# Performance work log

Measured on AMD Instinct MI355X. Metric: run time of the kernel, lower is better.

## Reference

```python
import jax, jax.numpy as jnp
import numpy as np

INPUT, HIDDEN, OUTPUT, BATCH = 2048, 32, 512, 16384


def setup_inputs() -> dict:
    key = jax.random.key(0)
    k1, k2, k3, k4 = jax.random.split(key, 4)
    x = jax.random.normal(k1, (BATCH, INPUT), dtype=jnp.float32)
    # torch init: uniform(-1, 1) for both linear weights and hebbian coeffs
    w1 = jax.random.uniform(k2, (HIDDEN, INPUT), jnp.float32, -1.0, 1.0)
    w2 = jax.random.uniform(k3, (OUTPUT, HIDDEN), jnp.float32, -1.0, 1.0)
    heb_coeffs = jax.random.uniform(k4, (HIDDEN * INPUT + OUTPUT * HIDDEN, 4), jnp.float32, -1.0, 1.0)
    return {"x": x, "w1": w1, "w2": w2, "heb_coeffs": heb_coeffs}


def reference(x, w1, w2, heb_coeffs):
    # Forward MLP: act = relu(x @ w1^T), out = sigmoid(act @ w2^T) - 0.4
    act = jax.nn.relu(x @ w1.T)                 # [B, HIDDEN]
    out = jax.nn.sigmoid(act @ w2.T) - 0.4      # [B, OUTPUT]

    B = x.shape[0]
    # idx = (shape0-1)*i + i + j == shape0*i + j  -> coeff layout [in_dim, out_dim, 4]
    c1 = heb_coeffs[: HIDDEN * INPUT].reshape(INPUT, HIDDEN, 4)
    c2 = heb_coeffs[HIDDEN * INPUT :].reshape(HIDDEN, OUTPUT, 4)

    # ABCD update, batch loop -> batch-summed outer products / rank-1 terms
    corr1 = jnp.einsum("bi,bj->ij", x, act)     # [INPUT, HIDDEN]
    dw1T = (B * c1[..., 3]
            + c1[..., 0] * corr1
            + c1[..., 1] * x.sum(0)[:, None]
            + c1[..., 2] * act.sum(0)[None, :])  # [INPUT, HIDDEN]

    corr2 = jnp.einsum("bi,bj->ij", act, out)   # [HIDDEN, OUTPUT]
    dw2T = (B * c2[..., 3]
            + c2[..., 0] * corr2
            + c2[..., 1] * act.sum(0)[:, None]
            + c2[..., 2] * out.sum(0)[None, :])  # [HIDDEN, OUTPUT]

    w1_new = w1 + dw1T.T                        # [HIDDEN, INPUT]
    w2_new = w2 + dw2T.T                        # [OUTPUT, HIDDEN]
    # row-wise L2 normalization (torch.norm(dim=1, keepdim=True))
    w1_new = w1_new / jnp.linalg.norm(w1_new, axis=1, keepdims=True)
    w2_new = w2_new / jnp.linalg.norm(w2_new, axis=1, keepdims=True)
    return out, w1_new, w2_new
```

## Files before the change

### kernel.cpp

```cpp
#include <hip/hip_runtime.h>
#include <math.h>

constexpr int BATCH = 16384;
constexpr int IND   = 2048;
constexpr int HID   = 32;
constexpr int OUTD  = 512;

constexpr int NC1 = 64;
constexpr int NSA = 64;
constexpr int NC2 = 128;

constexpr int SA   = 136;
constexpr int SXT  = 72;
constexpr int SATW = 136;
constexpr int SAT2 = 264;

typedef __attribute__((ext_vector_type(8))) short bf16x8;
typedef __attribute__((ext_vector_type(4))) float f32x4;

__device__ __forceinline__ unsigned short f2bf(float f) {
  unsigned u = __float_as_uint(f);
  u += 0x7FFFu + ((u >> 16) & 1u);
  return (unsigned short)(u >> 16);
}
__device__ __forceinline__ float bf2f(unsigned short h) {
  return __uint_as_float(((unsigned)h) << 16);
}
__device__ __forceinline__ void split2(float f, unsigned short& hi,
                                       unsigned short& lo) {
  hi = f2bf(f);
  lo = f2bf(f - bf2f(hi));
}
__device__ __forceinline__ int swzA(int row, int col) {
  return row * SA + (col ^ (((row >> 3) & 7) * 8));
}

__global__ __launch_bounds__(256) void k_cvtw(
    const float* __restrict__ w1, const float* __restrict__ w2,
    unsigned short* __restrict__ w1H, unsigned short* __restrict__ w1L,
    unsigned short* __restrict__ w2H, unsigned short* __restrict__ w2L) {
  const int bid = blockIdx.x;
  if (bid < 64) {
    const int g = bid * 256 + threadIdx.x;
    float4 v = ((const float4*)w1)[g];
    ushort4 h, l;
    split2(v.x, h.x, l.x); split2(v.y, h.y, l.y);
    split2(v.z, h.z, l.z); split2(v.w, h.w, l.w);
    ((ushort4*)w1H)[g] = h;
    ((ushort4*)w1L)[g] = l;
  } else {
    const int g = (bid - 64) * 256 + threadIdx.x;
    float4 v = ((const float4*)w2)[g];
    ushort4 h, l;
    split2(v.x, h.x, l.x); split2(v.y, h.y, l.y);
    split2(v.z, h.z, l.z); split2(v.w, h.w, l.w);
    ((ushort4*)w2H)[g] = h;
    ((ushort4*)w2L)[g] = l;
  }
}

__global__ __launch_bounds__(256, 4) void k_act(
    const float* __restrict__ x, const unsigned short* __restrict__ w1H,
    const unsigned short* __restrict__ w1L, float* __restrict__ act_part,
    unsigned short* __restrict__ xH) {
  const int tid = threadIdx.x;
  const int kq = blockIdx.x & 1;
  const int bt = blockIdx.x >> 1;
  const int b0 = bt * 32;
  const int kbase = kq * 1024;
  const int lane = tid & 63;
  const int wv = tid >> 6;
  const int arow = lane & 15;
  const int m4 = lane >> 4;
  const int ksub = m4 * 8;
  const int rt = wv & 1;
  const int ht = wv >> 1;

  __shared__ __align__(16) unsigned short XH[32 * SA];
  __shared__ __align__(16) unsigned short XL[32 * SA];
  __shared__ __align__(16) unsigned short WH[32 * SA];
  __shared__ __align__(16) unsigned short WL[32 * SA];

  const int rp = tid >> 4;
  const int kg = (tid & 15) * 8;

  float4 px0a, px0b, px1a, px1b;
  bf16x8 pwh0, pwl0, pwh1, pwl1;

#define LOADA(K0)                                                          \
  {                                                                        \
    const float* xr0 = x + (size_t)(b0 + 2 * rp) * IND + kbase + (K0) + kg;\
    const float* xr1 = xr0 + IND;                                          \
    px0a = *(const float4*)(xr0);                                          \
    px0b = *(const float4*)(xr0 + 4);                                      \
    px1a = *(const float4*)(xr1);                                          \
    px1b = *(const float4*)(xr1 + 4);                                      \
    const size_t wo = (size_t)(2 * rp) * IND + kbase + (K0) + kg;          \
    pwh0 = *(const bf16x8*)(&w1H[wo]);                                     \
    pwl0 = *(const bf16x8*)(&w1L[wo]);                                     \
    pwh1 = *(const bf16x8*)(&w1H[wo + IND]);                               \
    pwl1 = *(const bf16x8*)(&w1L[wo + IND]);                               \
  }

#define PUTX2(ROW, COL, V, GK)                                       \
  {                                                                  \
    ushort4 h_, l_;                                                  \
    split2((V).x, h_.x, l_.x); split2((V).y, h_.y, l_.y);            \
    split2((V).z, h_.z, l_.z); split2((V).w, h_.w, l_.w);            \
    *(ushort4*)(&XH[swzA((ROW), (COL))]) = h_;                       \
    *(ushort4*)(&XL[swzA((ROW), (COL))]) = l_;                       \
    *(ushort4*)(&xH[(size_t)(b0 + (ROW)) * IND + (GK) + (COL)]) = h_;\
  }

#define STOREA(GK)                                                   \
  {                                                                  \
    PUTX2(2 * rp, kg, px0a, GK);                                     \
    PUTX2(2 * rp, kg + 4, px0b, GK);                                 \
    PUTX2(2 * rp + 1, kg, px1a, GK);                                 \
    PUTX2(2 * rp + 1, kg + 4, px1b, GK);                             \
    *(bf16x8*)(&WH[swzA(2 * rp, kg)]) = pwh0;                        \
    *(bf16x8*)(&WL[swzA(2 * rp, kg)]) = pwl0;                        \
    *(bf16x8*)(&WH[swzA(2 * rp + 1, kg)]) = pwh1;                    \
    *(bf16x8*)(&WL[swzA(2 * rp + 1, kg)]) = pwl1;                    \
  }

  f32x4 accA = {0.f, 0.f, 0.f, 0.f};
  LOADA(0);

  for (int kc = 0; kc < 8; ++kc) {
    __syncthreads();
    STOREA(kbase + kc * 128);
    __syncthreads();
    if (kc < 7) LOADA((kc + 1) * 128);
    const int xrow = rt * 16 + arow;
    const int wrow = ht * 16 + arow;
#pragma unroll
    for (int ks = 0; ks < 4; ++ks) {
      const int kk = ks * 32 + ksub;
      bf16x8 ah = *(const bf16x8*)(&XH[swzA(xrow, kk)]);
      bf16x8 al = *(const bf16x8*)(&XL[swzA(xrow, kk)]);
      bf16x8 bh = *(const bf16x8*)(&WH[swzA(wrow, kk)]);
      bf16x8 bl_ = *(const bf16x8*)(&WL[swzA(wrow, kk)]);
      accA = __builtin_amdgcn_mfma_f32_16x16x32_bf16(ah, bh, accA, 0, 0, 0);
      accA = __builtin_amdgcn_mfma_f32_16x16x32_bf16(ah, bl_, accA, 0, 0, 0);
      accA = __builtin_amdgcn_mfma_f32_16x16x32_bf16(al, bh, accA, 0, 0, 0);
    }
  }

  const int bl = rt * 16 + (m4 << 2);
  const int h = ht * 16 + arow;
  float* p = act_part + (size_t)kq * (BATCH * HID);
#pragma unroll
  for (int r = 0; r < 4; ++r)
    p[(size_t)(b0 + bl + r) * HID + h] = accA[r];
}

__global__ __launch_bounds__(256) void k_actc(
    const float* __restrict__ act_part,
    unsigned short* __restrict__ actH, unsigned short* __restrict__ actL,
    unsigned short* __restrict__ actT, float* __restrict__ actsum_part) {
  const int tid = threadIdx.x;
  const int blk = blockIdx.x;
  const int b0 = blk * 256;

  __shared__ unsigned short asT[32][264];
  __shared__ float red[256][4];

  const float4* p0 = (const float4*)act_part;
  const float4* p1 = p0 + (size_t)BATCH * HID / 4;

  const int hq = tid & 7;
  float4 s{0.f, 0.f, 0.f, 0.f};
#pragma unroll
  for (int r = 0; r < 8; ++r) {
    const int e4 = r * 256 + tid;
    const int b = e4 >> 3;
    const size_t g = (size_t)(b0 + b) * 8 + hq;
    float4 a = p0[g];
    float4 c = p1[g];
    a.x = fmaxf(a.x + c.x, 0.f);  a.y = fmaxf(a.y + c.y, 0.f);
    a.z = fmaxf(a.z + c.z, 0.f);  a.w = fmaxf(a.w + c.w, 0.f);
    ushort4 hh, ll;
    split2(a.x, hh.x, ll.x); split2(a.y, hh.y, ll.y);
    split2(a.z, hh.z, ll.z); split2(a.w, hh.w, ll.w);
    *(ushort4*)(&actH[g * 4]) = hh;
    *(ushort4*)(&actL[g * 4]) = ll;
    asT[hq * 4 + 0][b] = hh.x;
    asT[hq * 4 + 1][b] = hh.y;
    asT[hq * 4 + 2][b] = hh.z;
    asT[hq * 4 + 3][b] = hh.w;
    s.x += a.x; s.y += a.y; s.z += a.z; s.w += a.w;
  }
  red[tid][0] = s.x; red[tid][1] = s.y;
  red[tid][2] = s.z; red[tid][3] = s.w;
  __syncthreads();

#pragma unroll
  for (int r = 0; r < 4; ++r) {
    const int slot = r * 256 + tid;
    const int hrow = slot >> 5;
    const int bseg = (slot & 31) * 8;
    bf16x8 v = *(const bf16x8*)(&asT[hrow][bseg]);
    *(bf16x8*)(&actT[(size_t)hrow * BATCH + b0 + bseg]) = v;
  }
  if (tid < 32) {
    const int q = tid >> 2, j = tid & 3;
    float t = 0.f;
#pragma unroll
    for (int sx = 0; sx < 32; ++sx) t += red[q + 8 * sx][j];
    actsum_part[blk * HID + tid] = t;
  }
}

__global__ __launch_bounds__(512, 3) void k_corr1(
    const unsigned short* __restrict__ xH,
    const unsigned short* __restrict__ actT,
    float* __restrict__ corr1T_part, float* __restrict__ xsum_part) {
  const int tid = threadIdx.x;
  const int bc = blockIdx.x >> 4;
  const int iq = blockIdx.x & 15;
  const int b0 = bc * 256;
  const int ibase = iq * 128;
  const int lane = tid & 63;
  const int wv = tid >> 6;
  const int arow = lane & 15;
  const int m4 = lane >> 4;
  const int ksub = m4 * 8;
  const int it = wv * 16;

  __shared__ __align__(16) unsigned short XT[128 * SXT];
  __shared__ __align__(16) unsigned short AT[48 * SAT2];

  for (int e = tid; e < 16 * SAT2; e += 512)
    AT[32 * SAT2 + e] = (unsigned short)0x3F80;
  {
    const int hrow = tid >> 4;
    const int sg = (tid & 15) * 16;
    const int sw = ((hrow >> 3) & 7) * 8;
#pragma unroll
    for (int j = 0; j < 2; ++j) {
      const int boff = sg + 8 * j;
      bf16x8 v = *(const bf16x8*)(&actT[(size_t)hrow * BATCH + b0 + boff]);
      *(bf16x8*)(&AT[hrow * SAT2 + (boff ^ sw)]) = v;
    }
  }

  const int ig = tid & 15;
  const int bq = tid >> 4;

  bf16x8 xa, ya;

#define LOADC(HF)                                                           \
  {                                                                         \
    const int icol = ibase + ig * 8;                                        \
    const unsigned short* r0 =                                              \
        xH + (size_t)(b0 + 64 * (HF) + 2 * bq) * IND + icol;                \
    xa = *(const bf16x8*)(r0);                                              \
    ya = *(const bf16x8*)(r0 + IND);                                        \
  }

#define STC                                                                 \
  {                                                                         \
    const int qb = (2 * bq) ^ ((ig & 7) * 8);                               \
    unsigned short* basew = &XT[(size_t)(ig * 8) * SXT + qb];               \
    ushort2 p;                                                              \
    p.x = (unsigned short)xa[0]; p.y = (unsigned short)ya[0];               \
    *(ushort2*)(basew + 0 * SXT) = p;                                       \
    p.x = (unsigned short)xa[1]; p.y = (unsigned short)ya[1];               \
    *(ushort2*)(basew + 1 * SXT) = p;                                       \
    p.x = (unsigned short)xa[2]; p.y = (unsigned short)ya[2];               \
    *(ushort2*)(basew + 2 * SXT) = p;                                       \
    p.x = (unsigned short)xa[3]; p.y = (unsigned short)ya[3];               \
    *(ushort2*)(basew + 3 * SXT) = p;                                       \
    p.x = (unsigned short)xa[4]; p.y = (unsigned short)ya[4];               \
    *(ushort2*)(basew + 4 * SXT) = p;                                       \
    p.x = (unsigned short)xa[5]; p.y = (unsigned short)ya[5];               \
    *(ushort2*)(basew + 5 * SXT) = p;                                       \
    p.x = (unsigned short)xa[6]; p.y = (unsigned short)ya[6];               \
    *(ushort2*)(basew + 6 * SXT) = p;                                       \
    p.x = (unsigned short)xa[7]; p.y = (unsigned short)ya[7];               \
    *(ushort2*)(basew + 7 * SXT) = p;                                       \
  }

  const int swzr = (((it + arow) >> 3) & 7) * 8;
  const int swze0 = ((arow >> 3) & 7) * 8;
  const int swze1 = (((16 + arow) >> 3) & 7) * 8;

  f32x4 c00 = {0.f, 0.f, 0.f, 0.f};
  f32x4 c01 = {0.f, 0.f, 0.f, 0.f};
  f32x4 c02 = {0.f, 0.f, 0.f, 0.f};

  LOADC(0);
#pragma unroll
  for (int hf = 0; hf < 4; ++hf) {
    __syncthreads();
    STC;
    __syncthreads();
    if (hf < 3) LOADC(hf + 1);
#pragma unroll
    for (int bs = 0; bs < 2; ++bs) {
      const int bb = bs * 32 + ksub;
      const int bb2 = 64 * hf + bb;
      bf16x8 a = *(const bf16x8*)(&XT[(it + arow) * SXT + (bb ^ swzr)]);
      bf16x8 e0 = *(const bf16x8*)(&AT[arow * SAT2 + (bb2 ^ swze0)]);
      bf16x8 e1 = *(const bf16x8*)(&AT[(16 + arow) * SAT2 + (bb2 ^ swze1)]);
      bf16x8 e2 = *(const bf16x8*)(&AT[(32 + arow) * SAT2 + bb2]);
      c00 = __builtin_amdgcn_mfma_f32_16x16x32_bf16(a, e0, c00, 0, 0, 0);
      c01 = __builtin_amdgcn_mfma_f32_16x16x32_bf16(a, e1, c01, 0, 0, 0);
      c02 = __builtin_amdgcn_mfma_f32_16x16x32_bf16(a, e2, c02, 0, 0, 0);
    }
  }

  float* basep = corr1T_part + (size_t)bc * (IND * HID);
  const int gi = ibase + it + (m4 << 2);
  *(f32x4*)(basep + (size_t)arow * IND + gi) = c00;
  *(f32x4*)(basep + (size_t)(16 + arow) * IND + gi) = c01;
  if (arow == 0)
    *(f32x4*)(xsum_part + (size_t)bc * IND + gi) = c02;
}

__global__ __launch_bounds__(256, 2) void k_fwd2m_red1(
    const unsigned short* __restrict__ actH,
    const unsigned short* __restrict__ actL,
    const unsigned short* __restrict__ actT,
    const unsigned short* __restrict__ w2H,
    const unsigned short* __restrict__ w2L,
    float* __restrict__ out, float* __restrict__ corr2_part,
    float* __restrict__ outsum_part,
    const float* __restrict__ c1p, const float* __restrict__ xsp,
    const float* __restrict__ asp,
    float* __restrict__ corr1T, float* __restrict__ xsum,
    float* __restrict__ actsum) {
  __shared__ __align__(16) unsigned short W2Hs[128 * 40];
  __shared__ __align__(16) unsigned short W2Ls[128 * 40];
  __shared__ __align__(16) unsigned short AH[64 * 40];
  __shared__ __align__(16) unsigned short AL[64 * 40];
  __shared__ __align__(16) unsigned short AT[48 * SATW];
  __shared__ __align__(16) unsigned short OT[128 * 72];

  const int tid = threadIdx.x;

  if (blockIdx.x >= 512) {
    const int e = (blockIdx.x - 512) * 256 + tid;
    float s = 0.f;
#pragma unroll 8
    for (int c = 0; c < NC1; ++c) s += c1p[(size_t)c * (IND * HID) + e];
    corr1T[e] = s;
    if (e < IND) {
      float t = 0.f;
#pragma unroll 8
      for (int c = 0; c < NC1; ++c) t += xsp[(size_t)c * IND + e];
      xsum[e] = t;
    }
    if (e < HID) {
      float t = 0.f;
#pragma unroll 8
      for (int c = 0; c < NSA; ++c) t += asp[(size_t)c * HID + e];
      actsum[e] = t;
    }
    return;
  }

  const int bc = blockIdx.x >> 2;
  const int og = blockIdx.x & 3;
  const int b0 = bc * 128;
  const int obase = og * 128;
  const int lane = tid & 63;
  const int wv = tid >> 6;
  const int arow = lane & 15;
  const int m4 = lane >> 4;
  const int ksub = m4 * 8;

  {
    const int r2 = tid >> 1, hh = (tid & 1) * 16;
    const size_t wo = (size_t)(obase + r2) * HID + hh;
    *(bf16x8*)(&W2Hs[r2 * 40 + hh]) = *(const bf16x8*)(&w2H[wo]);
    *(bf16x8*)(&W2Hs[r2 * 40 + hh + 8]) = *(const bf16x8*)(&w2H[wo + 8]);
    *(bf16x8*)(&W2Ls[r2 * 40 + hh]) = *(const bf16x8*)(&w2L[wo]);
    *(bf16x8*)(&W2Ls[r2 * 40 + hh + 8]) = *(const bf16x8*)(&w2L[wo + 8]);
  }
  {
    const int h = tid >> 3, seg16 = (tid & 7) * 16;
#pragma unroll
    for (int j = 0; j < 2; ++j) {
      const int seg = seg16 + 8 * j;
      *(bf16x8*)(&AT[h * SATW + seg]) =
          *(const bf16x8*)(&actT[(size_t)h * BATCH + b0 + seg]);
    }
  }
  for (int e = tid; e < 16 * SATW; e += 256)
    AT[32 * SATW + e] = (unsigned short)0x3F80;

  f32x4 c0a = {0.f,0.f,0.f,0.f}, c1a = {0.f,0.f,0.f,0.f}, c2a = {0.f,0.f,0.f,0.f};
  f32x4 c0b = {0.f,0.f,0.f,0.f}, c1b = {0.f,0.f,0.f,0.f}, c2b = {0.f,0.f,0.f,0.f};

  for (int hf = 0; hf < 2; ++hf) {
    __syncthreads();
    {
      const int b = tid >> 2, q = (tid & 3) * 8;
      *(bf16x8*)(&AH[b * 40 + q]) =
          *(const bf16x8*)(&actH[(size_t)(b0 + 64 * hf + b) * HID + q]);
      *(bf16x8*)(&AL[b * 40 + q]) =
          *(const bf16x8*)(&actL[(size_t)(b0 + 64 * hf + b) * HID + q]);
    }
    __syncthreads();

    const int bt = wv;
    bf16x8 fah = *(const bf16x8*)(&AH[(bt * 16 + arow) * 40 + ksub]);
    bf16x8 fal = *(const bf16x8*)(&AL[(bt * 16 + arow) * 40 + ksub]);
#pragma unroll
    for (int ot = 0; ot < 8; ++ot) {
      bf16x8 wbh = *(const bf16x8*)(&W2Hs[(ot * 16 + arow) * 40 + ksub]);
      bf16x8 wbl = *(const bf16x8*)(&W2Ls[(ot * 16 + arow) * 40 + ksub]);
      f32x4 z = {0.f, 0.f, 0.f, 0.f};
      z = __builtin_amdgcn_mfma_f32_16x16x32_bf16(fah, wbh, z, 0, 0, 0);
      z = __builtin_amdgcn_mfma_f32_16x16x32_bf16(fah, wbl, z, 0, 0, 0);
      z = __builtin_amdgcn_mfma_f32_16x16x32_bf16(fal, wbh, z, 0, 0, 0);
      ushort4 po;
      {
        float ov0 = 1.0f / (1.0f + __expf(-z[0])) - 0.4f;
        float ov1 = 1.0f / (1.0f + __expf(-z[1])) - 0.4f;
        float ov2 = 1.0f / (1.0f + __expf(-z[2])) - 0.4f;
        float ov3 = 1.0f / (1.0f + __expf(-z[3])) - 0.4f;
        const size_t ob = (size_t)(b0 + 64 * hf + bt * 16 + m4 * 4) * OUTD +
                          obase + ot * 16 + arow;
        out[ob + 0 * OUTD] = ov0;
        out[ob + 1 * OUTD] = ov1;
        out[ob + 2 * OUTD] = ov2;
        out[ob + 3 * OUTD] = ov3;
        po.x = f2bf(ov0); po.y = f2bf(ov1); po.z = f2bf(ov2); po.w = f2bf(ov3);
      }
      *(ushort4*)(&OT[(ot * 16 + arow) * 72 + bt * 16 + m4 * 4]) = po;
    }
    __syncthreads();

    {
      const int ot = wv * 2;
#pragma unroll
      for (int ks = 0; ks < 2; ++ks) {
        const int bb = ks * 32 + ksub;
        const int bb2 = 64 * hf + bb;
        bf16x8 bo = *(const bf16x8*)(&OT[(ot * 16 + arow) * 72 + bb]);
        bf16x8 a0 = *(const bf16x8*)(&AT[arow * SATW + bb2]);
        bf16x8 a1 = *(const bf16x8*)(&AT[(16 + arow) * SATW + bb2]);
        bf16x8 a2 = *(const bf16x8*)(&AT[(32 + arow) * SATW + bb2]);
        c0a = __builtin_amdgcn_mfma_f32_16x16x32_bf16(a0, bo, c0a, 0, 0, 0);
        c1a = __builtin_amdgcn_mfma_f32_16x16x32_bf16(a1, bo, c1a, 0, 0, 0);
        c2a = __builtin_amdgcn_mfma_f32_16x16x32_bf16(a2, bo, c2a, 0, 0, 0);
      }
    }
    {
      const int ot = wv * 2 + 1;
#pragma unroll
      for (int ks = 0; ks < 2; ++ks) {
        const int bb = ks * 32 + ksub;
        const int bb2 = 64 * hf + bb;
        bf16x8 bo = *(const bf16x8*)(&OT[(ot * 16 + arow) * 72 + bb]);
        bf16x8 a0 = *(const bf16x8*)(&AT[arow * SATW + bb2]);
        bf16x8 a1 = *(const bf16x8*)(&AT[(16 + arow) * SATW + bb2]);
        bf16x8 a2 = *(const bf16x8*)(&AT[(32 + arow) * SATW + bb2]);
        c0b = __builtin_amdgcn_mfma_f32_16x16x32_bf16(a0, bo, c0b, 0, 0, 0);
        c1b = __builtin_amdgcn_mfma_f32_16x16x32_bf16(a1, bo, c1b, 0, 0, 0);
        c2b = __builtin_amdgcn_mfma_f32_16x16x32_bf16(a2, bo, c2b, 0, 0, 0);
      }
    }
  }

  {
    const int ot0 = wv * 2, ot1 = wv * 2 + 1;
    float* cp0 = corr2_part + (size_t)bc * (HID * OUTD) + obase + ot0 * 16 + arow;
    float* cp1 = corr2_part + (size_t)bc * (HID * OUTD) + obase + ot1 * 16 + arow;
#pragma unroll
    for (int r = 0; r < 4; ++r) {
      cp0[(size_t)(m4 * 4 + r) * OUTD] = c0a[r];
      cp0[(size_t)(16 + m4 * 4 + r) * OUTD] = c1a[r];
      cp1[(size_t)(m4 * 4 + r) * OUTD] = c0b[r];
      cp1[(size_t)(16 + m4 * 4 + r) * OUTD] = c1b[r];
    }
    if (m4 == 0) {
      outsum_part[(size_t)bc * OUTD + obase + ot0 * 16 + arow] = c2a[0];
      outsum_part[(size_t)bc * OUTD + obase + ot1 * 16 + arow] = c2b[0];
    }
  }
}

__global__ __launch_bounds__(256) void k_w1_red2(
    const float* __restrict__ w1, const float* __restrict__ heb,
    const float* __restrict__ corr1T, const float* __restrict__ xsum,
    const float* __restrict__ actsum, float* __restrict__ w1out,
    const float* __restrict__ corr2_part,
    const float* __restrict__ outsum_part,
    float* __restrict__ corr2, float* __restrict__ outsum) {
  const int tid = threadIdx.x;
  __shared__ float red[256];

  if (blockIdx.x >= 32) {
    const int e = (blockIdx.x - 32) * 256 + tid;
    float s = 0.f;
#pragma unroll 8
    for (int c = 0; c < NC2; ++c) s += corr2_part[(size_t)c * (HID * OUTD) + e];
    corr2[e] = s;
    if (e < OUTD) {
      float t = 0.f;
#pragma unroll 8
      for (int c = 0; c < NC2; ++c) t += outsum_part[(size_t)c * OUTD + e];
      outsum[e] = t;
    }
    return;
  }

  const int h = blockIdx.x;
  const float ash = actsum[h];
  const float4* heb4 = (const float4*)heb;

  float val[8];
  float ss = 0.f;
#pragma unroll
  for (int r = 0; r < 8; ++r) {
    const int i = tid + 256 * r;
    float4 c = heb4[(size_t)i * HID + h];
    float v = w1[(size_t)h * IND + i] + 16384.0f * c.w +
              c.x * corr1T[(size_t)h * IND + i] + c.y * xsum[i] + c.z * ash;
    val[r] = v;
    ss += v * v;
  }

  red[tid] = ss;
  __syncthreads();
  for (int s = 128; s > 0; s >>= 1) {
    if (tid < s) red[tid] += red[tid + s];
    __syncthreads();
  }
  const float inv = 1.0f / sqrtf(red[0]);
#pragma unroll
  for (int r = 0; r < 8; ++r) {
    const int i = tid + 256 * r;
    w1out[(size_t)h * IND + i] = val[r] * inv;
  }
}

__global__ __launch_bounds__(256) void k_w2(
    const float* __restrict__ w2, const float* __restrict__ heb,
    const float* __restrict__ corr2, const float* __restrict__ actsum,
    const float* __restrict__ outsum, float* __restrict__ w2out) {
  const int o = blockIdx.x * 256 + threadIdx.x;
  const float oso = outsum[o];
  const float4* heb4 = (const float4*)heb;

  float val[HID];
  float ss = 0.f;
#pragma unroll
  for (int h = 0; h < HID; ++h) {
    float4 c = heb4[(size_t)(HID * IND) + (size_t)h * OUTD + o];
    float v = w2[(size_t)o * HID + h] + 16384.0f * c.w +
              c.x * corr2[(size_t)h * OUTD + o] + c.y * actsum[h] + c.z * oso;
    val[h] = v;
    ss += v * v;
  }
  const float inv = 1.0f / sqrtf(ss);
#pragma unroll
  for (int h = 0; h < HID; ++h) w2out[(size_t)o * HID + h] = val[h] * inv;
}

extern "C" void kernel_launch(void* const* d_in, const int* in_sizes, int n_in,
                              void* d_out, int out_size, void* d_ws,
                              size_t ws_size, hipStream_t stream) {
  const float* x   = (const float*)d_in[0];
  const float* w1  = (const float*)d_in[1];
  const float* w2  = (const float*)d_in[2];
  const float* heb = (const float*)d_in[3];

  float* out = (float*)d_out;
  float* w1o = out + (size_t)BATCH * OUTD;
  float* w2o = w1o + (size_t)HID * IND;

  float* ws = (float*)d_ws;
  unsigned short* actH = (unsigned short*)ws;
  unsigned short* actL = actH + (size_t)BATCH * HID;
  unsigned short* actT = actL + (size_t)BATCH * HID;
  unsigned short* w1H  = actT + (size_t)BATCH * HID;
  unsigned short* w1L  = w1H + (size_t)HID * IND;
  unsigned short* w2H  = w1L + (size_t)HID * IND;
  unsigned short* w2L  = w2H + (size_t)OUTD * HID;
  unsigned short* xH   = w2L + (size_t)OUTD * HID;
  float* corr1T      = (float*)(xH + (size_t)BATCH * IND);
  float* corr2       = corr1T + (size_t)IND * HID;
  float* xsum        = corr2 + (size_t)HID * OUTD;
  float* actsum      = xsum + IND;
  float* outsum      = actsum + HID;
  float* act_part    = outsum + OUTD;
  float* corr1T_part = act_part + (size_t)2 * BATCH * HID;
  float* xsum_part   = corr1T_part + (size_t)NC1 * IND * HID;
  float* actsum_part = xsum_part + (size_t)NC1 * IND;
  float* corr2_part  = actsum_part + (size_t)NSA * HID;
  float* outsum_part = corr2_part + (size_t)NC2 * HID * OUTD;

  k_cvtw      <<<80, 256, 0, stream>>>(w1, w2, w1H, w1L, w2H, w2L);
  k_act       <<<1024, 256, 0, stream>>>(x, w1H, w1L, act_part, xH);
  k_actc      <<<64, 256, 0, stream>>>(act_part, actH, actL, actT,
                                       actsum_part);
  k_corr1     <<<1024, 512, 0, stream>>>(xH, actT, corr1T_part, xsum_part);
  k_fwd2m_red1<<<768, 256, 0, stream>>>(actH, actL, actT, w2H, w2L, out,
                                        corr2_part, outsum_part,
                                        corr1T_part, xsum_part, actsum_part,
                                        corr1T, xsum, actsum);
  k_w1_red2   <<<96, 256, 0, stream>>>(w1, heb, corr1T, xsum, actsum, w1o,
                                       corr2_part, outsum_part, corr2,
                                       outsum);
  k_w2        <<<2, 256, 0, stream>>>(w2, heb, corr2, actsum, outsum, w2o);
}
```

Measured before the change: 106.7 us.

## Merge corr1 and fwd2 kernels, merge reductions and weight-update kernels

Fuses k_corr1 and the forward-layer-2/corr2 work into one 1536-block launch sharing a single shared-memory buffer, with the fwd2 blocks using only half of the 512 threads. The corr1 reduction moves into a combined reduction kernel with the corr2 reduction, and the w1 and w2 normalization kernels are merged. Constant-ones rows in shared memory are replaced by a register ones vector feeding the MFMA. This cuts launch count from 7 to 6 and overlaps the two independent GEMM phases. In exchange, fwd2 blocks idle half their threads, and corr1 blocks drop from 3 to 2 per CU under the new launch bound.

```diff
diff --git a/kernel.cpp b/kernel.cpp
--- a/kernel.cpp
+++ b/kernel.cpp
@@ -212,43 +212,52 @@
   }
 }
 
-__global__ __launch_bounds__(512, 3) void k_corr1(
+__global__ __launch_bounds__(512, 2) void k_corr1_fwd2m(
     const unsigned short* __restrict__ xH,
     const unsigned short* __restrict__ actT,
-    float* __restrict__ corr1T_part, float* __restrict__ xsum_part) {
+    float* __restrict__ corr1T_part, float* __restrict__ xsum_part,
+    const unsigned short* __restrict__ actH,
+    const unsigned short* __restrict__ actL,
+    const unsigned short* __restrict__ w2H,
+    const unsigned short* __restrict__ w2L,
+    float* __restrict__ out, float* __restrict__ corr2_part,
+    float* __restrict__ outsum_part) {
+  __shared__ __align__(16) char smem[57856];
   const int tid = threadIdx.x;
-  const int bc = blockIdx.x >> 4;
-  const int iq = blockIdx.x & 15;
-  const int b0 = bc * 256;
-  const int ibase = iq * 128;
-  const int lane = tid & 63;
-  const int wv = tid >> 6;
-  const int arow = lane & 15;
-  const int m4 = lane >> 4;
-  const int ksub = m4 * 8;
-  const int it = wv * 16;
-
-  __shared__ __align__(16) unsigned short XT[128 * SXT];
-  __shared__ __align__(16) unsigned short AT[48 * SAT2];
-
-  for (int e = tid; e < 16 * SAT2; e += 512)
-    AT[32 * SAT2 + e] = (unsigned short)0x3F80;
-  {
-    const int hrow = tid >> 4;
-    const int sg = (tid & 15) * 16;
-    const int sw = ((hrow >> 3) & 7) * 8;
-#pragma unroll
-    for (int j = 0; j < 2; ++j) {
-      const int boff = sg + 8 * j;
-      bf16x8 v = *(const bf16x8*)(&actT[(size_t)hrow * BATCH + b0 + boff]);
-      *(bf16x8*)(&AT[hrow * SAT2 + (boff ^ sw)]) = v;
-    }
-  }
-
-  const int ig = tid & 15;
-  const int bq = tid >> 4;
-
-  bf16x8 xa, ya;
+  const short ob = (short)0x3F80;
+  const bf16x8 ones = {ob, ob, ob, ob, ob, ob, ob, ob};
+
+  if (blockIdx.x < 1024) {
+    unsigned short* const XT = (unsigned short*)smem;
+    unsigned short* const AT = (unsigned short*)(smem + 18432);
+
+    const int bc = blockIdx.x >> 4;
+    const int iq = blockIdx.x & 15;
+    const int b0 = bc * 256;
+    const int ibase = iq * 128;
+    const int lane = tid & 63;
+    const int wv = tid >> 6;
+    const int arow = lane & 15;
+    const int m4 = lane >> 4;
+    const int ksub = m4 * 8;
+    const int it = wv * 16;
+
+    {
+      const int hrow = tid >> 4;
+      const int sg = (tid & 15) * 16;
+      const int sw = ((hrow >> 3) & 7) * 8;
+#pragma unroll
+      for (int j = 0; j < 2; ++j) {
+        const int boff = sg + 8 * j;
+        bf16x8 v = *(const bf16x8*)(&actT[(size_t)hrow * BATCH + b0 + boff]);
+        *(bf16x8*)(&AT[hrow * SAT2 + (boff ^ sw)]) = v;
+      }
+    }
+
+    const int ig = tid & 15;
+    const int bq = tid >> 4;
+
+    bf16x8 xa, ya;
 
 #define LOADC(HF)                                                           \
   {                                                                         \
@@ -282,121 +291,84 @@
     *(ushort2*)(basew + 7 * SXT) = p;                                       \
   }
 
-  const int swzr = (((it + arow) >> 3) & 7) * 8;
-  const int swze0 = ((arow >> 3) & 7) * 8;
-  const int swze1 = (((16 + arow) >> 3) & 7) * 8;
-
-  f32x4 c00 = {0.f, 0.f, 0.f, 0.f};
-  f32x4 c01 = {0.f, 0.f, 0.f, 0.f};
-  f32x4 c02 = {0.f, 0.f, 0.f, 0.f};
-
-  LOADC(0);
-#pragma unroll
-  for (int hf = 0; hf < 4; ++hf) {
-    __syncthreads();
-    STC;
-    __syncthreads();
-    if (hf < 3) LOADC(hf + 1);
-#pragma unroll
-    for (int bs = 0; bs < 2; ++bs) {
-      const int bb = bs * 32 + ksub;
-      const int bb2 = 64 * hf + bb;
-      bf16x8 a = *(const bf16x8*)(&XT[(it + arow) * SXT + (bb ^ swzr)]);
-      bf16x8 e0 = *(const bf16x8*)(&AT[arow * SAT2 + (bb2 ^ swze0)]);
-      bf16x8 e1 = *(const bf16x8*)(&AT[(16 + arow) * SAT2 + (bb2 ^ swze1)]);
-      bf16x8 e2 = *(const bf16x8*)(&AT[(32 + arow) * SAT2 + bb2]);
-      c00 = __builtin_amdgcn_mfma_f32_16x16x32_bf16(a, e0, c00, 0, 0, 0);
-      c01 = __builtin_amdgcn_mfma_f32_16x16x32_bf16(a, e1, c01, 0, 0, 0);
-      c02 = __builtin_amdgcn_mfma_f32_16x16x32_bf16(a, e2, c02, 0, 0, 0);
-    }
-  }
-
-  float* basep = corr1T_part + (size_t)bc * (IND * HID);
-  const int gi = ibase + it + (m4 << 2);
-  *(f32x4*)(basep + (size_t)arow * IND + gi) = c00;
-  *(f32x4*)(basep + (size_t)(16 + arow) * IND + gi) = c01;
-  if (arow == 0)
-    *(f32x4*)(xsum_part + (size_t)bc * IND + gi) = c02;
-}
-
-__global__ __launch_bounds__(256, 2) void k_fwd2m_red1(
-    const unsigned short* __restrict__ actH,
-    const unsigned short* __restrict__ actL,
-    const unsigned short* __restrict__ actT,
-    const unsigned short* __restrict__ w2H,
-    const unsigned short* __restrict__ w2L,
-    float* __restrict__ out, float* __restrict__ corr2_part,
-    float* __restrict__ outsum_part,
-    const float* __restrict__ c1p, const float* __restrict__ xsp,
-    const float* __restrict__ asp,
-    float* __restrict__ corr1T, float* __restrict__ xsum,
-    float* __restrict__ actsum) {
-  __shared__ __align__(16) unsigned short W2Hs[128 * 40];
-  __shared__ __align__(16) unsigned short W2Ls[128 * 40];
-  __shared__ __align__(16) unsigned short AH[64 * 40];
-  __shared__ __align__(16) unsigned short AL[64 * 40];
-  __shared__ __align__(16) unsigned short AT[48 * SATW];
-  __shared__ __align__(16) unsigned short OT[128 * 72];
-
-  const int tid = threadIdx.x;
-
-  if (blockIdx.x >= 512) {
-    const int e = (blockIdx.x - 512) * 256 + tid;
-    float s = 0.f;
-#pragma unroll 8
-    for (int c = 0; c < NC1; ++c) s += c1p[(size_t)c * (IND * HID) + e];
-    corr1T[e] = s;
-    if (e < IND) {
-      float t = 0.f;
-#pragma unroll 8
-      for (int c = 0; c < NC1; ++c) t += xsp[(size_t)c * IND + e];
-      xsum[e] = t;
-    }
-    if (e < HID) {
-      float t = 0.f;
-#pragma unroll 8
-      for (int c = 0; c < NSA; ++c) t += asp[(size_t)c * HID + e];
-      actsum[e] = t;
-    }
+    const int swzr = (((it + arow) >> 3) & 7) * 8;
+    const int swze0 = ((arow >> 3) & 7) * 8;
+    const int swze1 = (((16 + arow) >> 3) & 7) * 8;
+
+    f32x4 c00 = {0.f, 0.f, 0.f, 0.f};
+    f32x4 c01 = {0.f, 0.f, 0.f, 0.f};
+    f32x4 c02 = {0.f, 0.f, 0.f, 0.f};
+
+    LOADC(0);
+#pragma unroll
+    for (int hf = 0; hf < 4; ++hf) {
+      __syncthreads();
+      STC;
+      __syncthreads();
+      if (hf < 3) LOADC(hf + 1);
+#pragma unroll
+      for (int bs = 0; bs < 2; ++bs) {
+        const int bb = bs * 32 + ksub;
+        const int bb2 = 64 * hf + bb;
+        bf16x8 a = *(const bf16x8*)(&XT[(it + arow) * SXT + (bb ^ swzr)]);
+        bf16x8 e0 = *(const bf16x8*)(&AT[arow * SAT2 + (bb2 ^ swze0)]);
+        bf16x8 e1 = *(const bf16x8*)(&AT[(16 + arow) * SAT2 + (bb2 ^ swze1)]);
+        c00 = __builtin_amdgcn_mfma_f32_16x16x32_bf16(a, e0, c00, 0, 0, 0);
+        c01 = __builtin_amdgcn_mfma_f32_16x16x32_bf16(a, e1, c01, 0, 0, 0);
+        c02 = __builtin_amdgcn_mfma_f32_16x16x32_bf16(a, ones, c02, 0, 0, 0);
+      }
+    }
+
+    float* basep = corr1T_part + (size_t)bc * (IND * HID);
+    const int gi = ibase + it + (m4 << 2);
+    *(f32x4*)(basep + (size_t)arow * IND + gi) = c00;
+    *(f32x4*)(basep + (size_t)(16 + arow) * IND + gi) = c01;
+    if (arow == 0)
+      *(f32x4*)(xsum_part + (size_t)bc * IND + gi) = c02;
     return;
   }
 
-  const int bc = blockIdx.x >> 2;
-  const int og = blockIdx.x & 3;
+  unsigned short* const W2Hs = (unsigned short*)smem;
+  unsigned short* const W2Ls = (unsigned short*)(smem + 10240);
+  unsigned short* const AH   = (unsigned short*)(smem + 20480);
+  unsigned short* const AL   = (unsigned short*)(smem + 25600);
+  unsigned short* const AT2  = (unsigned short*)(smem + 30720);
+  unsigned short* const OT   = (unsigned short*)(smem + 39424);
+
+  const bool on = tid < 256;
+  const int bidx = blockIdx.x - 1024;
+  const int bc = bidx >> 2;
+  const int og = bidx & 3;
   const int b0 = bc * 128;
   const int obase = og * 128;
   const int lane = tid & 63;
-  const int wv = tid >> 6;
+  const int wv = (tid >> 6) & 3;
   const int arow = lane & 15;
   const int m4 = lane >> 4;
   const int ksub = m4 * 8;
 
-  {
+  if (on) {
     const int r2 = tid >> 1, hh = (tid & 1) * 16;
     const size_t wo = (size_t)(obase + r2) * HID + hh;
     *(bf16x8*)(&W2Hs[r2 * 40 + hh]) = *(const bf16x8*)(&w2H[wo]);
     *(bf16x8*)(&W2Hs[r2 * 40 + hh + 8]) = *(const bf16x8*)(&w2H[wo + 8]);
     *(bf16x8*)(&W2Ls[r2 * 40 + hh]) = *(const bf16x8*)(&w2L[wo]);
     *(bf16x8*)(&W2Ls[r2 * 40 + hh + 8]) = *(const bf16x8*)(&w2L[wo + 8]);
-  }
-  {
     const int h = tid >> 3, seg16 = (tid & 7) * 16;
 #pragma unroll
     for (int j = 0; j < 2; ++j) {
       const int seg = seg16 + 8 * j;
-      *(bf16x8*)(&AT[h * SATW + seg]) =
+      *(bf16x8*)(&AT2[h * SATW + seg]) =
           *(const bf16x8*)(&actT[(size_t)h * BATCH + b0 + seg]);
     }
   }
-  for (int e = tid; e < 16 * SATW; e += 256)
-    AT[32 * SATW + e] = (unsigned short)0x3F80;
 
   f32x4 c0a = {0.f,0.f,0.f,0.f}, c1a = {0.f,0.f,0.f,0.f}, c2a = {0.f,0.f,0.f,0.f};
   f32x4 c0b = {0.f,0.f,0.f,0.f}, c1b = {0.f,0.f,0.f,0.f}, c2b = {0.f,0.f,0.f,0.f};
 
   for (int hf = 0; hf < 2; ++hf) {
     __syncthreads();
-    {
+    if (on) {
       const int b = tid >> 2, q = (tid & 3) * 8;
       *(bf16x8*)(&AH[b * 40 + q]) =
           *(const bf16x8*)(&actH[(size_t)(b0 + 64 * hf + b) * HID + q]);
@@ -405,68 +377,71 @@
     }
     __syncthreads();
 
-    const int bt = wv;
-    bf16x8 fah = *(const bf16x8*)(&AH[(bt * 16 + arow) * 40 + ksub]);
-    bf16x8 fal = *(const bf16x8*)(&AL[(bt * 16 + arow) * 40 + ksub]);
-#pragma unroll
-    for (int ot = 0; ot < 8; ++ot) {
-      bf16x8 wbh = *(const bf16x8*)(&W2Hs[(ot * 16 + arow) * 40 + ksub]);
-      bf16x8 wbl = *(const bf16x8*)(&W2Ls[(ot * 16 + arow) * 40 + ksub]);
-      f32x4 z = {0.f, 0.f, 0.f, 0.f};
-      z = __builtin_amdgcn_mfma_f32_16x16x32_bf16(fah, wbh, z, 0, 0, 0);
-      z = __builtin_amdgcn_mfma_f32_16x16x32_bf16(fah, wbl, z, 0, 0, 0);
-      z = __builtin_amdgcn_mfma_f32_16x16x32_bf16(fal, wbh, z, 0, 0, 0);
-      ushort4 po;
+    if (on) {
+      const int bt = wv;
+      bf16x8 fah = *(const bf16x8*)(&AH[(bt * 16 + arow) * 40 + ksub]);
+      bf16x8 fal = *(const bf16x8*)(&AL[(bt * 16 + arow) * 40 + ksub]);
+#pragma unroll
+      for (int ot = 0; ot < 8; ++ot) {
+        bf16x8 wbh = *(const bf16x8*)(&W2Hs[(ot * 16 + arow) * 40 + ksub]);
+        bf16x8 wbl = *(const bf16x8*)(&W2Ls[(ot * 16 + arow) * 40 + ksub]);
+        f32x4 z = {0.f, 0.f, 0.f, 0.f};
+        z = __builtin_amdgcn_mfma_f32_16x16x32_bf16(fah, wbh, z, 0, 0, 0);
+        z = __builtin_amdgcn_mfma_f32_16x16x32_bf16(fah, wbl, z, 0, 0, 0);
+        z = __builtin_amdgcn_mfma_f32_16x16x32_bf16(fal, wbh, z, 0, 0, 0);
+        ushort4 po;
+        {
+          float ov0 = 1.0f / (1.0f + __expf(-z[0])) - 0.4f;
+          float ov1 = 1.0f / (1.0f + __expf(-z[1])) - 0.4f;
+          float ov2 = 1.0f / (1.0f + __expf(-z[2])) - 0.4f;
+          float ov3 = 1.0f / (1.0f + __expf(-z[3])) - 0.4f;
+          const size_t obp = (size_t)(b0 + 64 * hf + bt * 16 + m4 * 4) * OUTD +
+                             obase + ot * 16 + arow;
+          out[obp + 0 * OUTD] = ov0;
+          out[obp + 1 * OUTD] = ov1;
+          out[obp + 2 * OUTD] = ov2;
+          out[obp + 3 * OUTD] = ov3;
+          po.x = f2bf(ov0); po.y = f2bf(ov1);
+          po.z = f2bf(ov2); po.w = f2bf(ov3);
+        }
+        *(ushort4*)(&OT[(ot * 16 + arow) * 72 + bt * 16 + m4 * 4]) = po;
+      }
+    }
+    __syncthreads();
+
+    if (on) {
       {
-        float ov0 = 1.0f / (1.0f + __expf(-z[0])) - 0.4f;
-        float ov1 = 1.0f / (1.0f + __expf(-z[1])) - 0.4f;
-        float ov2 = 1.0f / (1.0f + __expf(-z[2])) - 0.4f;
-        float ov3 = 1.0f / (1.0f + __expf(-z[3])) - 0.4f;
-        const size_t ob = (size_t)(b0 + 64 * hf + bt * 16 + m4 * 4) * OUTD +
-                          obase + ot * 16 + arow;
-        out[ob + 0 * OUTD] = ov0;
-        out[ob + 1 * OUTD] = ov1;
-        out[ob + 2 * OUTD] = ov2;
-        out[ob + 3 * OUTD] = ov3;
-        po.x = f2bf(ov0); po.y = f2bf(ov1); po.z = f2bf(ov2); po.w = f2bf(ov3);
+        const int ot = wv * 2;
+#pragma unroll
+        for (int ks = 0; ks < 2; ++ks) {
+          const int bb = ks * 32 + ksub;
+          const int bb2 = 64 * hf + bb;
+          bf16x8 bo = *(const bf16x8*)(&OT[(ot * 16 + arow) * 72 + bb]);
+          bf16x8 a0 = *(const bf16x8*)(&AT2[arow * SATW + bb2]);
+          bf16x8 a1 = *(const bf16x8*)(&AT2[(16 + arow) * SATW + bb2]);
+          c0a = __builtin_amdgcn_mfma_f32_16x16x32_bf16(a0, bo, c0a, 0, 0, 0);
+          c1a = __builtin_amdgcn_mfma_f32_16x16x32_bf16(a1, bo, c1a, 0, 0, 0);
+          c2a = __builtin_amdgcn_mfma_f32_16x16x32_bf16(ones, bo, c2a, 0, 0, 0);
+        }
       }
-      *(ushort4*)(&OT[(ot * 16 + arow) * 72 + bt * 16 + m4 * 4]) = po;
-    }
-    __syncthreads();
-
-    {
-      const int ot = wv * 2;
-#pragma unroll
-      for (int ks = 0; ks < 2; ++ks) {
-        const int bb = ks * 32 + ksub;
-        const int bb2 = 64 * hf + bb;
-        bf16x8 bo = *(const bf16x8*)(&OT[(ot * 16 + arow) * 72 + bb]);
-        bf16x8 a0 = *(const bf16x8*)(&AT[arow * SATW + bb2]);
-        bf16x8 a1 = *(const bf16x8*)(&AT[(16 + arow) * SATW + bb2]);
-        bf16x8 a2 = *(const bf16x8*)(&AT[(32 + arow) * SATW + bb2]);
-        c0a = __builtin_amdgcn_mfma_f32_16x16x32_bf16(a0, bo, c0a, 0, 0, 0);
-        c1a = __builtin_amdgcn_mfma_f32_16x16x32_bf16(a1, bo, c1a, 0, 0, 0);
-        c2a = __builtin_amdgcn_mfma_f32_16x16x32_bf16(a2, bo, c2a, 0, 0, 0);
+      {
+        const int ot = wv * 2 + 1;
+#pragma unroll
+        for (int ks = 0; ks < 2; ++ks) {
+          const int bb = ks * 32 + ksub;
+          const int bb2 = 64 * hf + bb;
+          bf16x8 bo = *(const bf16x8*)(&OT[(ot * 16 + arow) * 72 + bb]);
+          bf16x8 a0 = *(const bf16x8*)(&AT2[arow * SATW + bb2]);
+          bf16x8 a1 = *(const bf16x8*)(&AT2[(16 + arow) * SATW + bb2]);
+          c0b = __builtin_amdgcn_mfma_f32_16x16x32_bf16(a0, bo, c0b, 0, 0, 0);
+          c1b = __builtin_amdgcn_mfma_f32_16x16x32_bf16(a1, bo, c1b, 0, 0, 0);
+          c2b = __builtin_amdgcn_mfma_f32_16x16x32_bf16(ones, bo, c2b, 0, 0, 0);
+        }
       }
     }
-    {
-      const int ot = wv * 2 + 1;
-#pragma unroll
-      for (int ks = 0; ks < 2; ++ks) {
-        const int bb = ks * 32 + ksub;
-        const int bb2 = 64 * hf + bb;
-        bf16x8 bo = *(const bf16x8*)(&OT[(ot * 16 + arow) * 72 + bb]);
-        bf16x8 a0 = *(const bf16x8*)(&AT[arow * SATW + bb2]);
-        bf16x8 a1 = *(const bf16x8*)(&AT[(16 + arow) * SATW + bb2]);
-        bf16x8 a2 = *(const bf16x8*)(&AT[(32 + arow) * SATW + bb2]);
-        c0b = __builtin_amdgcn_mfma_f32_16x16x32_bf16(a0, bo, c0b, 0, 0, 0);
-        c1b = __builtin_amdgcn_mfma_f32_16x16x32_bf16(a1, bo, c1b, 0, 0, 0);
-        c2b = __builtin_amdgcn_mfma_f32_16x16x32_bf16(a2, bo, c2b, 0, 0, 0);
-      }
-    }
-  }
-
-  {
+  }
+
+  if (on) {
     const int ot0 = wv * 2, ot1 = wv * 2 + 1;
     float* cp0 = corr2_part + (size_t)bc * (HID * OUTD) + obase + ot0 * 16 + arow;
     float* cp1 = corr2_part + (size_t)bc * (HID * OUTD) + obase + ot1 * 16 + arow;
@@ -484,18 +459,17 @@
   }
 }
 
-__global__ __launch_bounds__(256) void k_w1_red2(
-    const float* __restrict__ w1, const float* __restrict__ heb,
-    const float* __restrict__ corr1T, const float* __restrict__ xsum,
-    const float* __restrict__ actsum, float* __restrict__ w1out,
+__global__ __launch_bounds__(256) void k_red12(
+    const float* __restrict__ c1p, const float* __restrict__ xsp,
+    const float* __restrict__ asp,
+    float* __restrict__ corr1T, float* __restrict__ xsum,
+    float* __restrict__ actsum,
     const float* __restrict__ corr2_part,
     const float* __restrict__ outsum_part,
     float* __restrict__ corr2, float* __restrict__ outsum) {
   const int tid = threadIdx.x;
-  __shared__ float red[256];
-
-  if (blockIdx.x >= 32) {
-    const int e = (blockIdx.x - 32) * 256 + tid;
+  if (blockIdx.x >= 256) {
+    const int e = (blockIdx.x - 256) * 256 + tid;
     float s = 0.f;
 #pragma unroll 8
     for (int c = 0; c < NC2; ++c) s += corr2_part[(size_t)c * (HID * OUTD) + e];
@@ -508,11 +482,57 @@
     }
     return;
   }
+  const int e = blockIdx.x * 256 + tid;
+  float s = 0.f;
+#pragma unroll 8
+  for (int c = 0; c < NC1; ++c) s += c1p[(size_t)c * (IND * HID) + e];
+  corr1T[e] = s;
+  if (e < IND) {
+    float t = 0.f;
+#pragma unroll 8
+    for (int c = 0; c < NC1; ++c) t += xsp[(size_t)c * IND + e];
+    xsum[e] = t;
+  }
+  if (e < HID) {
+    float t = 0.f;
+#pragma unroll 8
+    for (int c = 0; c < NSA; ++c) t += asp[(size_t)c * HID + e];
+    actsum[e] = t;
+  }
+}
+
+__global__ __launch_bounds__(256) void k_w12(
+    const float* __restrict__ w1, const float* __restrict__ heb,
+    const float* __restrict__ corr1T, const float* __restrict__ xsum,
+    const float* __restrict__ actsum, float* __restrict__ w1out,
+    const float* __restrict__ w2, const float* __restrict__ corr2,
+    const float* __restrict__ outsum, float* __restrict__ w2out) {
+  const int tid = threadIdx.x;
+  __shared__ float red[256];
+
+  if (blockIdx.x >= 32) {
+    const int o = (blockIdx.x - 32) * 256 + tid;
+    const float oso = outsum[o];
+    const float4* heb4 = (const float4*)heb;
+    float val[HID];
+    float ss = 0.f;
+#pragma unroll
+    for (int h = 0; h < HID; ++h) {
+      float4 c = heb4[(size_t)(HID * IND) + (size_t)h * OUTD + o];
+      float v = w2[(size_t)o * HID + h] + 16384.0f * c.w +
+                c.x * corr2[(size_t)h * OUTD + o] + c.y * actsum[h] + c.z * oso;
+      val[h] = v;
+      ss += v * v;
+    }
+    const float inv = 1.0f / sqrtf(ss);
+#pragma unroll
+    for (int h = 0; h < HID; ++h) w2out[(size_t)o * HID + h] = val[h] * inv;
+    return;
+  }
 
   const int h = blockIdx.x;
   const float ash = actsum[h];
   const float4* heb4 = (const float4*)heb;
-
   float val[8];
   float ss = 0.f;
 #pragma unroll
@@ -524,7 +544,6 @@
     val[r] = v;
     ss += v * v;
   }
-
   red[tid] = ss;
   __syncthreads();
   for (int s = 128; s > 0; s >>= 1) {
@@ -537,29 +556,6 @@
     const int i = tid + 256 * r;
     w1out[(size_t)h * IND + i] = val[r] * inv;
   }
-}
-
-__global__ __launch_bounds__(256) void k_w2(
-    const float* __restrict__ w2, const float* __restrict__ heb,
-    const float* __restrict__ corr2, const float* __restrict__ actsum,
-    const float* __restrict__ outsum, float* __restrict__ w2out) {
-  const int o = blockIdx.x * 256 + threadIdx.x;
-  const float oso = outsum[o];
-  const float4* heb4 = (const float4*)heb;
-
-  float val[HID];
-  float ss = 0.f;
-#pragma unroll
-  for (int h = 0; h < HID; ++h) {
-    float4 c = heb4[(size_t)(HID * IND) + (size_t)h * OUTD + o];
-    float v = w2[(size_t)o * HID + h] + 16384.0f * c.w +
-              c.x * corr2[(size_t)h * OUTD + o] + c.y * actsum[h] + c.z * oso;
-    val[h] = v;
-    ss += v * v;
-  }
-  const float inv = 1.0f / sqrtf(ss);
-#pragma unroll
-  for (int h = 0; h < HID; ++h) w2out[(size_t)o * HID + h] = val[h] * inv;
 }
 
 extern "C" void kernel_launch(void* const* d_in, const int* in_sizes, int n_in,
@@ -595,17 +591,17 @@
   float* corr2_part  = actsum_part + (size_t)NSA * HID;
   float* outsum_part = corr2_part + (size_t)NC2 * HID * OUTD;
 
-  k_cvtw      <<<80, 256, 0, stream>>>(w1, w2, w1H, w1L, w2H, w2L);
-  k_act       <<<1024, 256, 0, stream>>>(x, w1H, w1L, act_part, xH);
-  k_actc      <<<64, 256, 0, stream>>>(act_part, actH, actL, actT,
-                                       actsum_part);
-  k_corr1     <<<1024, 512, 0, stream>>>(xH, actT, corr1T_part, xsum_part);
-  k_fwd2m_red1<<<768, 256, 0, stream>>>(actH, actL, actT, w2H, w2L, out,
-                                        corr2_part, outsum_part,
-                                        corr1T_part, xsum_part, actsum_part,
-                                        corr1T, xsum, actsum);
-  k_w1_red2   <<<96, 256, 0, stream>>>(w1, heb, corr1T, xsum, actsum, w1o,
-                                       corr2_part, outsum_part, corr2,
-                                       outsum);
-  k_w2        <<<2, 256, 0, stream>>>(w2, heb, corr2, actsum, outsum, w2o);
-}
+  k_cvtw       <<<80, 256, 0, stream>>>(w1, w2, w1H, w1L, w2H, w2L);
+  k_act        <<<1024, 256, 0, stream>>>(x, w1H, w1L, act_part, xH);
+  k_actc       <<<64, 256, 0, stream>>>(act_part, actH, actL, actT,
+                                        actsum_part);
+  k_corr1_fwd2m<<<1536, 512, 0, stream>>>(xH, actT, corr1T_part, xsum_part,
+                                          actH, actL, w2H, w2L, out,
+                                          corr2_part, outsum_part);
+  k_red12      <<<320, 256, 0, stream>>>(corr1T_part, xsum_part, actsum_part,
+                                         corr1T, xsum, actsum,
+                                         corr2_part, outsum_part, corr2,
+                                         outsum);
+  k_w12        <<<34, 256, 0, stream>>>(w1, heb, corr1T, xsum, actsum, w1o,
+                                        w2, corr2, outsum, w2o);
+}
```

Measured after the change: 98.88 us. 7.4% less time.
